# Performance work log

Measured on AMD Instinct MI355X. Metric: run time of the kernel, lower is better.

Reference implementation:

```python
import jax, jax.numpy as jnp
import numpy as np

NUM_GROUPS = 64
TOPK = 8
BLOCK_M = 128
NUM_TOKENS = 8192
HIDDEN = 4096


def _build_perm(flat_ids_np, num_groups, block_m):
    """Single-pass histogram + stable sort + per-expert padding.

    Returns sorted_token_ids (int64, [total_padded]) and m_indices (int32,
    [total_padded]) exactly matching the torch per-expert loop semantics:
    each expert's slot list padded to a multiple of block_m by repeating its
    last slot (or zeros for empty experts).
    Output length is data-dependent, so this runs on host numpy (concrete
    values), mirroring the original module whose output shape is also
    data-dependent.
    """
    n = flat_ids_np.shape[0]
    order = np.argsort(flat_ids_np, kind="stable")  # token slots grouped by expert
    counts = np.bincount(flat_ids_np, minlength=num_groups)
    padded = (counts + block_m - 1) // block_m * block_m
    in_starts = np.concatenate([[0], np.cumsum(counts)])
    out_starts = np.concatenate([[0], np.cumsum(padded)])
    total = int(out_starts[-1])
    sorted_token_ids = np.zeros(total, dtype=np.int64)
    m_indices = np.zeros(total, dtype=np.int32)
    for e in range(num_groups):  # fixed small expert count
        c, p, o = int(counts[e]), int(padded[e]), int(out_starts[e])
        m_indices[o:o + p] = e
        if c > 0:
            seg = order[int(in_starts[e]):int(in_starts[e]) + c]
            sorted_token_ids[o:o + c] = seg
            sorted_token_ids[o + c:o + p] = seg[-1]  # pad with last slot
        # empty expert: rows stay zero (matches torch.zeros branch)
    np.clip(sorted_token_ids, None, n - 1, out=sorted_token_ids)
    return sorted_token_ids, m_indices


def setup_inputs() -> dict:
    key = jax.random.key(0)
    k1, k2 = jax.random.split(key)
    hidden_states = jax.random.normal(k1, (NUM_TOKENS, HIDDEN), dtype=jnp.bfloat16)
    topk_ids = jax.random.randint(k2, (NUM_TOKENS, TOPK), 0, NUM_GROUPS, dtype=jnp.int32)
    return {"hidden_states": hidden_states, "topk_ids": topk_ids}


def reference(hidden_states, topk_ids):
    m, _ = hidden_states.shape
    num_flat = m * TOPK
    flat_ids = np.asarray(topk_ids).reshape(-1)
    sorted_token_ids_np, m_indices_np = _build_perm(flat_ids, NUM_GROUPS, BLOCK_M)
    sorted_token_ids = jnp.asarray(sorted_token_ids_np)
    m_indices = jnp.asarray(m_indices_np)
    # inverse permutation for later unpermute (stable argsort breaks pad ties deterministically)
    inv_perm = jnp.argsort(sorted_token_ids, stable=True)[:num_flat]
    source_token_idx = sorted_token_ids // TOPK  # expert-contiguous gather indices
    output = hidden_states[source_token_idx]     # [total_padded, HIDDEN] bf16 gather
    return output, m_indices, inv_perm
```

## Files before the change

### kernel.cpp

```cpp
#include <hip/hip_runtime.h>
#include <hip/hip_bf16.h>

#define NG 64
#define TOPK 8
#define BM 128
#define NSLOT 65536
#define HID 4096
#define NTOK 8192
#define NSEG 64

typedef unsigned int v4u __attribute__((ext_vector_type(4)));
typedef unsigned int v2u __attribute__((ext_vector_type(2)));


__global__ __launch_bounds__(256) void hist_scan_k(const int* __restrict__ ids,
                                                   int* __restrict__ ws) {
    __shared__ int h[NG], lm[NG];
    __shared__ int winner;
    int t = threadIdx.x, s = blockIdx.x;
    if (t < NG) { h[t] = 0; lm[t] = -1; }
    __syncthreads();
    int base = s * 1024;
    for (int i = t; i < 1024; i += 256) {
        int e = ids[base + i] & (NG - 1);
        atomicAdd(&h[e], 1);
        atomicMax(&lm[e], base + i);
    }
    __syncthreads();
    if (t < NG) {
        ws[320 + t * 64 + s] = h[t];
        ws[4416 + t * 64 + s] = lm[t];
    }
    __threadfence();
    __syncthreads();
    if (t == 0) {
        unsigned old = atomicAdd((unsigned*)&ws[257], 1u);
        winner = ((old & 63u) == 63u) ? 1 : 0;
    }
    __syncthreads();
    if (!winner) return;
    __threadfence();
    if (t < NG) {
        int e = t, c = 0, last = -1;
        for (int b = 0; b < NSEG; b++) {
            c += ws[320 + e * 64 + b];
            int l = ws[4416 + e * 64 + b];
            last = l > last ? l : last;
        }
        ws[64 + e] = c;
        ws[128 + e] = (c + BM - 1) / BM * BM;
        ws[192 + e] = last;
    }
    __syncthreads();
    if (t == 0) {
        int acc = 0;
        for (int f = 0; f < NG; f++) { ws[f] = acc; acc += ws[128 + f]; }
        ws[256] = acc;
    }
}

__global__ __launch_bounds__(64) void rank_k(const int* __restrict__ ids,
                                             const int* __restrict__ ws,
                                             unsigned short* __restrict__ rank) {
    int s = blockIdx.x;
    int lane = threadIdx.x;
    int base = 0;
    for (int s2 = 0; s2 < s; s2++) base += ws[320 + lane * 64 + s2];
    int segbase = s * 1024;
    unsigned long long below = (1ULL << lane) - 1ULL;
    for (int c0 = 0; c0 < 1024; c0 += 64) {
        int e = ids[segbase + c0 + lane] & (NG - 1);
        int r = 0;
#pragma unroll 8
        for (int x = 0; x < NG; x++) {
            unsigned long long m = __ballot(e == x);
            if (m) {
                int bx = __shfl(base, x);
                if (e == x) r = bx + __popcll(m & below);
                if (lane == x) base += (int)__popcll(m);
            }
        }
        rank[segbase + c0 + lane] = (unsigned short)r;
    }
}

__global__ __launch_bounds__(256) void copy_k(const __hip_bfloat16* __restrict__ hs,
                                              const int* __restrict__ ids,
                                              const int* __restrict__ ws,
                                              const unsigned short* __restrict__ rank,
                                              float* __restrict__ out) {
    __shared__ int s_last[NG], s_pad[NG];
    int b = blockIdx.x;
    int total = ws[256];
    int t = threadIdx.x;
    float* m_out = out + (size_t)total * HID;
    if (b < NTOK) {
        const v2u* s2 = (const v2u*)(hs + (size_t)b * HID);
        v4u a[4];
#pragma unroll
        for (int q = 0; q < 4; q++) {
            v2u w = s2[t + 256 * q];
            a[q].x = w.x << 16; a[q].y = w.x & 0xFFFF0000u;
            a[q].z = w.y << 16; a[q].w = w.y & 0xFFFF0000u;
        }
        int slot0 = b * TOPK;
#pragma unroll
        for (int k = 0; k < TOPK; k++) {
            int e = ids[slot0 + k] & (NG - 1);
            int dst = ws[e] + (int)rank[slot0 + k];
            if (dst < 0 || dst >= total) continue;
            v4u* d = (v4u*)(out + (size_t)dst * HID);
#pragma unroll
            for (int q = 0; q < 4; q++) d[t + 256 * q] = a[q];
            if (t == 0) m_out[dst] = (float)e;
        }
    } else if (b < NTOK + NG * BM) {
        int q0 = b - NTOK;
        int e = q0 >> 7;
        int j = q0 & 127;
        int c = ws[64 + e], p = ws[128 + e];
        if (c + j >= p) return;
        int srcslot = ws[192 + e];
        int dst = ws[e] + c + j;
        if (dst < 0 || dst >= total) return;
        int src = srcslot >> 3;
        if (src < 0 || src >= NTOK) return;
        if (t == 0) m_out[dst] = (float)e;
        const v2u* s2 = (const v2u*)(hs + (size_t)src * HID);
        v4u* d = (v4u*)(out + (size_t)dst * HID);
#pragma unroll
        for (int q = 0; q < 4; q++) {
            v2u w = s2[t + 256 * q];
            v4u a = {w.x << 16, w.x & 0xFFFF0000u, w.y << 16, w.y & 0xFFFF0000u};
            d[t + 256 * q] = a;
        }
    } else {
        if (t < NG) {
            s_last[t] = ws[192 + t];
            s_pad[t] = ws[128 + t] - ws[64 + t];
        }
        __syncthreads();
        float* inv_out = out + (size_t)total * (HID + 1);
        int i = (b - NTOK - NG * BM) * 256 + t;
        int e = ids[i] & (NG - 1);
        int pos = ws[e] + (int)rank[i];
        int base = i;
#pragma unroll
        for (int f = 0; f < NG; f++) {
            int l = s_last[f];
            base += (l >= 0 && l < i) ? s_pad[f] : 0;
        }
        if (base < NSLOT) inv_out[base] = (float)pos;
        if (i == s_last[e]) {
            int oc = ws[e] + ws[64 + e];
            int pd = s_pad[e];
            for (int j = 0; j < pd; j++) {
                int idx = base + 1 + j;
                if (idx >= NSLOT) break;
                inv_out[idx] = (float)(oc + j);
            }
        }
    }
}

extern "C" void kernel_launch(void* const* d_in, const int* in_sizes, int n_in,
                              void* d_out, int out_size, void* d_ws, size_t ws_size,
                              hipStream_t stream) {
    const __hip_bfloat16* hs = (const __hip_bfloat16*)d_in[0];
    const int* ids = (const int*)d_in[1];
    float* out = (float*)d_out;

    int* ws = (int*)d_ws;
    unsigned short* rank = (unsigned short*)(ws + 8704);

    hipLaunchKernelGGL(hist_scan_k, dim3(NSEG), dim3(256), 0, stream, ids, ws);
    hipLaunchKernelGGL(rank_k, dim3(NSEG), dim3(64), 0, stream, ids, ws, rank);
    hipLaunchKernelGGL(copy_k, dim3(NTOK + NG * BM + NSLOT / 256), dim3(256), 0, stream,
                       hs, ids, ws, rank, out);
}
```

Before: 298.5 us.

## Fuse histogram, scan and rank into one kernel with grid-wide spin barrier

Merges the histogram/scan kernel and the rank kernel into a single prep kernel of 128 wavefronts, each handling 512 slots. Per-segment counts and last-slot indices come from ballot loops, and a global atomic counter acts as a spin barrier so one wave can finish the totals with a shuffle-based prefix scan. Every wave then ranks its own ids from registers. This removes a kernel launch and the second read of ids. In exchange it depends on all 32 blocks being resident at once for the spin barrier, adds a memset, and moves the rank buffer offset.

Measured after the change: 301.1 us. No clear change (+0.9%).

```diff
diff --git a/kernel.cpp b/kernel.cpp
--- a/kernel.cpp
+++ b/kernel.cpp
@@ -7,80 +7,87 @@
 #define NSLOT 65536
 #define HID 4096
 #define NTOK 8192
-#define NSEG 64
+#define NSEG 128
+#define NWAVE 128
 
 typedef unsigned int v4u __attribute__((ext_vector_type(4)));
 typedef unsigned int v2u __attribute__((ext_vector_type(2)));
 
 
-__global__ __launch_bounds__(256) void hist_scan_k(const int* __restrict__ ids,
-                                                   int* __restrict__ ws) {
-    __shared__ int h[NG], lm[NG];
-    __shared__ int winner;
-    int t = threadIdx.x, s = blockIdx.x;
-    if (t < NG) { h[t] = 0; lm[t] = -1; }
-    __syncthreads();
-    int base = s * 1024;
-    for (int i = t; i < 1024; i += 256) {
-        int e = ids[base + i] & (NG - 1);
-        atomicAdd(&h[e], 1);
-        atomicMax(&lm[e], base + i);
+__global__ __launch_bounds__(256) void prep_k(const int* __restrict__ ids,
+                                              int* __restrict__ ws,
+                                              unsigned short* __restrict__ rank) {
+    int lane = threadIdx.x & 63;
+    int s = blockIdx.x * 4 + (threadIdx.x >> 6);
+    int segbase = s * 512;
+    unsigned long long below = (1ULL << lane) - 1ULL;
+
+    int myid[8];
+#pragma unroll
+    for (int c = 0; c < 8; c++) myid[c] = ids[segbase + c * 64 + lane] & (NG - 1);
+    int cnt = 0, lastm = -1;
+#pragma unroll
+    for (int c = 0; c < 8; c++) {
+        int id = myid[c];
+#pragma unroll 8
+        for (int x = 0; x < NG; x++) {
+            unsigned long long m = __ballot(id == x);
+            if (m && lane == x) {
+                cnt += (int)__popcll(m);
+                lastm = segbase + c * 64 + (63 - __builtin_clzll(m));
+            }
+        }
     }
-    __syncthreads();
-    if (t < NG) {
-        ws[320 + t * 64 + s] = h[t];
-        ws[4416 + t * 64 + s] = lm[t];
+    ws[320 + lane * NSEG + s] = cnt;
+    ws[8512 + lane * NSEG + s] = lastm;
+    __threadfence();
+
+    int win = 0;
+    if (lane == 0) {
+        unsigned old = atomicAdd((unsigned*)&ws[257], 1u);
+        win = (old == NWAVE - 1) ? 1 : 0;
+        while (__hip_atomic_load((unsigned*)&ws[257], __ATOMIC_RELAXED,
+                                 __HIP_MEMORY_SCOPE_AGENT) < NWAVE) {}
     }
+    win = __shfl(win, 0);
     __threadfence();
-    __syncthreads();
-    if (t == 0) {
-        unsigned old = atomicAdd((unsigned*)&ws[257], 1u);
-        winner = ((old & 63u) == 63u) ? 1 : 0;
-    }
-    __syncthreads();
-    if (!winner) return;
-    __threadfence();
-    if (t < NG) {
-        int e = t, c = 0, last = -1;
-        for (int b = 0; b < NSEG; b++) {
-            c += ws[320 + e * 64 + b];
-            int l = ws[4416 + e * 64 + b];
+
+    if (win) {
+        int c = 0, last = -1;
+        for (int b2 = 0; b2 < NSEG; b2++) {
+            c += ws[320 + lane * NSEG + b2];
+            int l = ws[8512 + lane * NSEG + b2];
             last = l > last ? l : last;
         }
-        ws[64 + e] = c;
-        ws[128 + e] = (c + BM - 1) / BM * BM;
-        ws[192 + e] = last;
+        int p = (c + BM - 1) / BM * BM;
+        ws[64 + lane] = c;
+        ws[128 + lane] = p;
+        ws[192 + lane] = last;
+        int acc = p;
+        for (int off = 1; off < 64; off <<= 1) {
+            int v = __shfl_up(acc, off);
+            if (lane >= off) acc += v;
+        }
+        ws[lane] = acc - p;
+        if (lane == 63) ws[256] = acc;
     }
-    __syncthreads();
-    if (t == 0) {
-        int acc = 0;
-        for (int f = 0; f < NG; f++) { ws[f] = acc; acc += ws[128 + f]; }
-        ws[256] = acc;
-    }
-}
 
-__global__ __launch_bounds__(64) void rank_k(const int* __restrict__ ids,
-                                             const int* __restrict__ ws,
-                                             unsigned short* __restrict__ rank) {
-    int s = blockIdx.x;
-    int lane = threadIdx.x;
     int base = 0;
-    for (int s2 = 0; s2 < s; s2++) base += ws[320 + lane * 64 + s2];
-    int segbase = s * 1024;
-    unsigned long long below = (1ULL << lane) - 1ULL;
-    for (int c0 = 0; c0 < 1024; c0 += 64) {
-        int e = ids[segbase + c0 + lane] & (NG - 1);
+    for (int s2 = 0; s2 < s; s2++) base += ws[320 + lane * NSEG + s2];
+#pragma unroll
+    for (int c = 0; c < 8; c++) {
+        int id = myid[c];
         int r = 0;
 #pragma unroll 8
         for (int x = 0; x < NG; x++) {
-            unsigned long long m = __ballot(e == x);
+            unsigned long long m = __ballot(id == x);
             if (m) {
                 int bx = __shfl(base, x);
-                if (e == x) r = bx + __popcll(m & below);
+                if (id == x) r = bx + __popcll(m & below);
                 if (lane == x) base += (int)__popcll(m);
             }
         }
-        rank[segbase + c0 + lane] = (unsigned short)r;
+        rank[segbase + c * 64 + lane] = (unsigned short)r;
     }
 }
 
@@ -171,10 +178,10 @@
     float* out = (float*)d_out;
 
     int* ws = (int*)d_ws;
-    unsigned short* rank = (unsigned short*)(ws + 8704);
+    unsigned short* rank = (unsigned short*)(ws + 16704);
 
-    hipLaunchKernelGGL(hist_scan_k, dim3(NSEG), dim3(256), 0, stream, ids, ws);
-    hipLaunchKernelGGL(rank_k, dim3(NSEG), dim3(64), 0, stream, ids, ws, rank);
+    hipMemsetAsync((void*)(ws + 257), 0, sizeof(int), stream);
+    hipLaunchKernelGGL(prep_k, dim3(32), dim3(256), 0, stream, ids, ws, rank);
     hipLaunchKernelGGL(copy_k, dim3(NTOK + NG * BM + NSLOT / 256), dim3(256), 0, stream,
                        hs, ids, ws, rank, out);
 }
```
